# Kernel optimization log

Hardware: AMD Instinct MI355X
Metric: run time of the kernel (lower is better)

## Reference

```python
import jax, jax.numpy as jnp
import numpy as np

D = 512      # input_size == per-head embed_size (wide attention)
H = 8        # num_attn_heads


def setup_inputs() -> dict:
    key = jax.random.key(0)
    ks = jax.random.split(key, 8)
    B, S = 2, 2048
    scale = 1.0 / np.sqrt(D)
    return {
        "Xin_q": jax.random.normal(ks[0], (B, S, D), dtype=jnp.float32),
        "Xin_k": jax.random.normal(ks[1], (B, S, D), dtype=jnp.float32),
        "Xin_v": jax.random.normal(ks[2], (B, S, D), dtype=jnp.float32),
        # per-head projection weights, stored as [H, D_in, D_out] (bias-free)
        "Wq": jax.random.normal(ks[3], (H, D, D), dtype=jnp.float32) * scale,
        "Wk": jax.random.normal(ks[4], (H, D, D), dtype=jnp.float32) * scale,
        "Wv": jax.random.normal(ks[5], (H, D, D), dtype=jnp.float32) * scale,
        # output projection: concat(H*D) -> D, with bias
        "Wz": jax.random.normal(ks[6], (H * D, D), dtype=jnp.float32) * (1.0 / np.sqrt(H * D)),
        "bz": jax.random.normal(ks[7], (D,), dtype=jnp.float32) * 0.01,
    }


def reference(Xin_q, Xin_k, Xin_v, Wq, Wk, Wv, Wz, bz):
    B, Sq, _ = Xin_q.shape
    inv4 = 1.0 / (D ** 0.25)  # each of Q and K scaled by embed_size**(1/4)
    # project all heads at once: [B,H,S,D]
    q = jnp.einsum("bsd,hde->bhse", Xin_q, Wq) * inv4
    k = jnp.einsum("bsd,hde->bhse", Xin_k, Wk) * inv4
    v = jnp.einsum("bsd,hde->bhse", Xin_v, Wv)
    attn = jax.nn.softmax(jnp.einsum("bhqe,bhke->bhqk", q, k), axis=-1)
    z = jnp.einsum("bhqk,bhke->bhqe", attn, v)        # [B,H,S,D]
    # concat heads along last dim (head-major order matches torch.cat over the head loop)
    z = jnp.transpose(z, (0, 2, 1, 3)).reshape(B, Sq, H * D)
    out = z @ Wz + bz                                  # [B,S,D]
    attn_avg = jnp.mean(attn, axis=1)                  # [B,Sq,Skv]
    return out, attn_avg
```

## Files before the change

kernel.cpp:

```cpp
#include <hip/hip_runtime.h>
#include <math.h>

#define BB 2
#define SS 2048
#define D_ 512
#define H_ 8
#define MS (BB * SS)
#define HD (H_ * D_)

typedef short bf16x8 __attribute__((ext_vector_type(8)));
typedef float f32x4 __attribute__((ext_vector_type(4)));

__device__ inline unsigned short f2bf(float f) {
    union { float f; unsigned u; } x{f};
    unsigned r = x.u + 0x7fff + ((x.u >> 16) & 1);
    return (unsigned short)(r >> 16);
}
__device__ inline float bf2f(unsigned short u) {
    union { unsigned u; float f; } x{(unsigned)u << 16};
    return x.f;
}

constexpr size_t SZ_X   = (size_t)MS * D_ * 2;
constexpr size_t SZ_W   = (size_t)H_ * D_ * D_ * 2;
constexpr size_t SZ_WZ  = (size_t)HD * D_ * 2;
constexpr size_t SZ_QK  = (size_t)H_ * MS * D_ * 2;
constexpr size_t SZ_SC  = (size_t)H_ * BB * SS * SS * 2;
constexpr size_t SZ_Z   = (size_t)MS * HD * 2;
constexpr size_t SZ_OP  = (size_t)2 * MS * D_ * 4;
constexpr size_t SZ_LV  = (size_t)H_ * BB * SS * 4;
constexpr size_t OFF_XQ  = 0;
constexpr size_t OFF_XK  = OFF_XQ + SZ_X;
constexpr size_t OFF_XV  = OFF_XK + SZ_X;
constexpr size_t OFF_WQT = OFF_XV + SZ_X;
constexpr size_t OFF_WKT = OFF_WQT + SZ_W;
constexpr size_t OFF_WVT = OFF_WKT + SZ_W;
constexpr size_t OFF_WZT = OFF_WVT + SZ_W;
constexpr size_t OFF_QB  = OFF_WZT + SZ_WZ;
constexpr size_t OFF_KB  = OFF_QB + SZ_QK;
constexpr size_t OFF_VT  = OFF_KB + SZ_QK;
constexpr size_t OFF_SC  = OFF_VT + SZ_QK;
constexpr size_t OFF_Z   = OFF_SC + SZ_SC;
constexpr size_t OFF_OP  = OFF_Z + SZ_Z;
constexpr size_t OFF_LV  = OFF_OP + SZ_OP;
constexpr size_t WS_TOTAL = OFF_LV + SZ_LV;
__device__ __align__(256) unsigned char g_ws[WS_TOTAL];

__device__ inline void gl2lds16(const unsigned short* g, unsigned short* l) {
    __builtin_amdgcn_global_load_lds(
        (const __attribute__((address_space(1))) void*)g,
        (__attribute__((address_space(3))) void*)l, 16, 0, 0);
}

#define BAR() __builtin_amdgcn_s_barrier()
#define PRIO1() __builtin_amdgcn_s_setprio(1)
#define PRIO0() __builtin_amdgcn_s_setprio(0)
#define SCHED0() __builtin_amdgcn_sched_barrier(0)
#define VMW4() asm volatile("s_waitcnt vmcnt(4)" ::: "memory")
#define VMW0() asm volatile("s_waitcnt vmcnt(0)" ::: "memory")

__device__ __forceinline__ void rd_a(const unsigned short* p, int qm, int o0, int o1,
                                     bf16x8 (&Af)[8]) {
#pragma unroll
    for (int fi = 0; fi < 4; fi++) {
        Af[2 * fi]     = *(const bf16x8*)(p + (qm * 64 + fi * 16) * 64 + o0);
        Af[2 * fi + 1] = *(const bf16x8*)(p + (qm * 64 + fi * 16) * 64 + o1);
    }
}
__device__ __forceinline__ void rd_b(const unsigned short* p, int qn, int o0, int o1,
                                     bf16x8 (&Bf)[4]) {
#pragma unroll
    for (int fj = 0; fj < 2; fj++) {
        const int t = qn * 2 + fj;
        Bf[2 * fj]     = *(const bf16x8*)(p + t * 64 + o0);
        Bf[2 * fj + 1] = *(const bf16x8*)(p + t * 64 + o1);
    }
}
__device__ __forceinline__ void mma_q(int qm, int qn, const bf16x8 (&Af)[8],
                                      const bf16x8 (&Bf)[4], f32x4 (&acc)[8][4]) {
#pragma unroll
    for (int fi = 0; fi < 4; fi++)
#pragma unroll
        for (int fj = 0; fj < 2; fj++) {
            acc[qm * 4 + fi][qn * 2 + fj] = __builtin_amdgcn_mfma_f32_16x16x32_bf16(
                Af[2 * fi], Bf[2 * fj], acc[qm * 4 + fi][qn * 2 + fj], 0, 0, 0);
            acc[qm * 4 + fi][qn * 2 + fj] = __builtin_amdgcn_mfma_f32_16x16x32_bf16(
                Af[2 * fi + 1], Bf[2 * fj + 1], acc[qm * 4 + fi][qn * 2 + fj], 0, 0, 0);
        }
}

__global__ __launch_bounds__(512, 2) void gemm256_k(
    const unsigned short* __restrict__ A, const unsigned short* __restrict__ B,
    unsigned short* __restrict__ C, int K, int ldA, int ldB, int ldC,
    long sA1, long sA2, long sB1, long sB2, long sC1, long sC2, int d2,
    float alpha, int doExp, const float* __restrict__ rowScale, long sR1, long sR2,
    int gx, int gy, int gz)
{
    __shared__ unsigned short LA[2][256 * 64];
    __shared__ unsigned short LB[2][256 * 64];
    const int tid = threadIdx.x;
    const int w = tid >> 6, l = tid & 63;
    const int wm = w >> 2, wn = w & 3;

    const int sr = l >> 3;
    const int sqA = (l & 7) ^ sr;
    const int sqB0 = (l & 7) ^ ((w * 4 + (sr >> 2)) & 7);
    const int sqB1 = sqB0 ^ 2;
    const int q = l >> 4, sl = l & 7;
    const int o0 = (q ^ sl) * 8;
    const int o1 = ((q + 4) ^ sl) * 8;
    const unsigned short* pa0 = &LA[0][(wm * 128 + (l & 15)) * 64];
    const unsigned short* pa1 = &LA[1][(wm * 128 + (l & 15)) * 64];
    const unsigned short* pb0 = &LB[0][(wn * 64 + (l & 15) * 4) * 64];
    const unsigned short* pb1 = &LB[1][(wn * 64 + (l & 15) * 4) * 64];

    const int tilesPerZ = gx * gy;
    const int zPerXcd = gz >> 3;
    const int perXcd = zPerXcd * tilesPerZ;
    const int xcd = blockIdx.x & 7, jj = blockIdx.x >> 3;
    const int nT = (perXcd - jj + 31) >> 5;
    const int nK2 = K >> 7;

    auto decode = [&](int idx, const unsigned short*& gA,
                      const unsigned short*& gB0, const unsigned short*& gB1,
                      long& cO, long& rO, int& m0o, int& n0o) {
        const int zl = idx / tilesPerZ;
        const int rem = idx - zl * tilesPerZ;
        const int by = rem / gx;
        const int bx = rem - by * gx;
        const int bz = xcd * zPerXcd + zl;
        const int z1 = bz / d2, z2 = bz - z1 * d2;
        m0o = by * 256; n0o = bx * 256;
        const unsigned short* Az = A + z1 * sA1 + z2 * sA2;
        const unsigned short* Bz = B + z1 * sB1 + z2 * sB2;
        gA  = Az + (long)(m0o + w * 16 + sr) * ldA + sqA * 8;
        gB0 = Bz + (long)(n0o + w * 16 + sr) * ldB + sqB0 * 8;
        gB1 = Bz + (long)(n0o + w * 16 + 8 + sr) * ldB + sqB1 * 8;
        cO = z1 * sC1 + z2 * sC2;
        rO = z1 * sR1 + z2 * sR2;
    };

    const unsigned short *gAc, *gB0c, *gB1c, *gAn, *gB0n, *gB1n;
    long cOff, rsOff, cOffN, rsOffN;
    int m0, n0, m0N, n0N;
    decode(jj, gAc, gB0c, gB1c, cOff, rsOff, m0, n0);
    gAn = gAc; gB0n = gB0c; gB1n = gB1c;
    cOffN = cOff; rsOffN = rsOff; m0N = m0; n0N = n0;

    f32x4 acc[8][4] = {};
    bf16x8 Af[8], Bf0[4], Bf1[4];

#define STG_A(bufi, half, base, t) do { \
    gl2lds16((base) + (long)((half) * 128) * ldA + (long)(t) * 64, \
             &LA[bufi][((half) * 128 + w * 16) * 64]); \
    gl2lds16((base) + (long)((half) * 128 + 8) * ldA + (long)(t) * 64, \
             &LA[bufi][((half) * 128 + w * 16 + 8) * 64]); } while (0)
#define STG_B(bufi, half, b0, b1, t) do { \
    gl2lds16((b0) + (long)((half) * 128) * ldB + (long)(t) * 64, \
             &LB[bufi][((half) * 128 + w * 16) * 64]); \
    gl2lds16((b1) + (long)((half) * 128) * ldB + (long)(t) * 64, \
             &LB[bufi][((half) * 128 + w * 16 + 8) * 64]); } while (0)

    STG_A(0, 0, gAc, 0); STG_A(0, 1, gAc, 0);
    STG_B(0, 0, gB0c, gB1c, 0); STG_B(0, 1, gB0c, gB1c, 0);
    STG_B(1, 0, gB0c, gB1c, 1); STG_B(1, 1, gB0c, gB1c, 1);
    VMW4();
    BAR();
    SCHED0();

    for (int k = 0; k < nT; ++k) {
        const bool hasNext = (k + 1 < nT);
        if (hasNext) decode(jj + (k + 1) * 32, gAn, gB0n, gB1n,
                            cOffN, rsOffN, m0N, n0N);

        for (int u = 0; u < nK2; ++u) {
            const int t1 = 2 * u + 1, t2 = 2 * u + 2, t3 = 2 * u + 3;
            const bool lastU = (u == nK2 - 1);
            const bool stg = !lastU || hasNext;
            const unsigned short* a2 = lastU ? gAn : gAc;
            const unsigned short* b20 = lastU ? gB0n : gB0c;
            const unsigned short* b21 = lastU ? gB1n : gB1c;
            const int tt2 = lastU ? 0 : t2;
            const int tt3 = lastU ? 1 : t3;
            rd_a(pa0, 0, o0, o1, Af);
            rd_b(pb0, 0, o0, o1, Bf0);
            STG_A(1, 0, gAc, t1);
            PRIO1(); mma_q(0, 0, Af, Bf0, acc); PRIO0(); BAR();
            rd_b(pb0, 1, o0, o1, Bf1);
            STG_A(1, 1, gAc, t1);
            PRIO1(); mma_q(0, 1, Af, Bf1, acc); PRIO0(); BAR();
            rd_a(pa0, 1, o0, o1, Af);
            if (stg) STG_B(0, 0, b20, b21, tt2);
            PRIO1(); mma_q(1, 1, Af, Bf1, acc); PRIO0(); BAR();
            if (stg) STG_B(0, 1, b20, b21, tt2);
            PRIO1(); mma_q(1, 0, Af, Bf0, acc); PRIO0();
            if (stg) VMW4(); else VMW0();
            BAR();
            SCHED0();
            rd_a(pa1, 0, o0, o1, Af);
            rd_b(pb1, 0, o0, o1, Bf0);
            if (stg) STG_A(0, 0, a2, tt2);
            PRIO1(); mma_q(0, 0, Af, Bf0, acc); PRIO0(); BAR();
            rd_b(pb1, 1, o0, o1, Bf1);
            if (stg) STG_A(0, 1, a2, tt2);
            PRIO1(); mma_q(0, 1, Af, Bf1, acc); PRIO0(); BAR();
            rd_a(pa1, 1, o0, o1, Af);
            if (stg) STG_B(1, 0, b20, b21, tt3);
            PRIO1(); mma_q(1, 1, Af, Bf1, acc); PRIO0(); BAR();
            if (stg) STG_B(1, 1, b20, b21, tt3);
            PRIO1(); mma_q(1, 0, Af, Bf0, acc); PRIO0();
            if (stg) VMW4(); else VMW0();
            BAR();
            SCHED0();
        }

        {
            const int rowB = m0 + wm * 128 + q * 4;
            const int colB = n0 + wn * 64 + (l & 15) * 4;
            unsigned short* Cp = C + cOff;
#pragma unroll
            for (int mi = 0; mi < 8; mi++) {
#pragma unroll
                for (int rg = 0; rg < 4; rg++) {
                    const int row = rowB + mi * 16 + rg;
                    const float rs = rowScale ? rowScale[rsOff + row] : 1.0f;
                    float v0 = alpha * acc[mi][0][rg];
                    float v1 = alpha * acc[mi][1][rg];
                    float v2 = alpha * acc[mi][2][rg];
                    float v3 = alpha * acc[mi][3][rg];
                    if (doExp) {
                        v0 = __expf(v0); v1 = __expf(v1);
                        v2 = __expf(v2); v3 = __expf(v3);
                    }
                    uint2 pk;
                    pk.x = (unsigned)f2bf(v0 * rs) | ((unsigned)f2bf(v1 * rs) << 16);
                    pk.y = (unsigned)f2bf(v2 * rs) | ((unsigned)f2bf(v3 * rs) << 16);
                    *(uint2*)(Cp + (long)row * ldC + colB) = pk;
                }
            }
        }
#pragma unroll
        for (int mi = 0; mi < 8; mi++)
#pragma unroll
            for (int nj = 0; nj < 4; nj++)
                acc[mi][nj] = (f32x4){0.f, 0.f, 0.f, 0.f};
        gAc = gAn; gB0c = gB0n; gB1c = gB1n;
        cOff = cOffN; rsOff = rsOffN; m0 = m0N; n0 = n0N;
    }
#undef STG_A
#undef STG_B
}

__global__ __launch_bounds__(256) void gemm_bt_k(
    const unsigned short* __restrict__ A, const unsigned short* __restrict__ B,
    void* __restrict__ Cv, int K, int ldA, int ldB, int ldC,
    long sA1, long sA2, long sB1, long sB2, long sC1, long sC2, int d2,
    float alpha, const float* __restrict__ bias, int outBf16, int doExp,
    const float* __restrict__ rowScale, long sR1, long sR2)
{
    __shared__ unsigned short As[128 * 64];
    __shared__ unsigned short Bs[128 * 64];
    const int gx = gridDim.x, gy = gridDim.y, gz = gridDim.z;
    int bx, by, bz;
    if (((gy * gz) & 7) == 0) {
        const long L = blockIdx.x + (long)gx * (blockIdx.y + (long)gy * blockIdx.z);
        const int d = (int)(L & 7);
        const long s = L >> 3;
        bx = (int)(s % gx);
        const long yz = d + 8 * (s / gx);
        by = (int)(yz % gy);
        bz = (int)(yz / gy);
    } else {
        bx = blockIdx.x; by = blockIdx.y; bz = blockIdx.z;
    }
    const int z1 = bz / d2, z2 = bz % d2;
    A += z1 * sA1 + z2 * sA2;
    B += z1 * sB1 + z2 * sB2;
    const long cOff = z1 * sC1 + z2 * sC2;
    const long rsOff = z1 * sR1 + z2 * sR2;
    const int m0 = by * 128, n0 = bx * 128;
    const int tid = threadIdx.x;
    const int w = tid >> 6, l = tid & 63;

    const int sr = l >> 3;
    const int sq = (l & 7) ^ sr;
    const unsigned short* ga = A + (long)(m0 + w * 32 + sr) * ldA + sq * 8;
    const unsigned short* gb = B + (long)(n0 + w * 32 + sr) * ldB + sq * 8;
    unsigned short* laA = As + w * 2048;
    unsigned short* laB = Bs + w * 2048;

    const int wm = w >> 1, wn = w & 1;
    const int q = l >> 4;
    const int sl = l & 7;
    const int mA = wm * 64 + (l & 15);
    const int nB = wn * 64 + (l & 15);
    const int s0 = ((q) ^ sl) * 8;
    const int s1 = ((q + 4) ^ sl) * 8;
    const unsigned short* pa0 = As + mA * 64 + s0;
    const unsigned short* pa1 = As + mA * 64 + s1;
    const unsigned short* pb0 = Bs + nB * 64 + s0;
    const unsigned short* pb1 = Bs + nB * 64 + s1;

    f32x4 acc[4][4] = {};
    for (int kk = 0; kk < K; kk += 64) {
#pragma unroll
        for (int i = 0; i < 4; i++) {
            gl2lds16(ga + (long)i * 8 * ldA, laA + i * 512);
            gl2lds16(gb + (long)i * 8 * ldB, laB + i * 512);
        }
        ga += 64; gb += 64;
        __syncthreads();
        bf16x8 af[4], bf[4];
#pragma unroll
        for (int i = 0; i < 4; i++) {
            af[i] = *(const bf16x8*)(pa0 + i * 1024);
            bf[i] = *(const bf16x8*)(pb0 + i * 1024);
        }
#pragma unroll
        for (int mi = 0; mi < 4; mi++)
#pragma unroll
            for (int ni = 0; ni < 4; ni++)
                acc[mi][ni] = __builtin_amdgcn_mfma_f32_16x16x32_bf16(
                    af[mi], bf[ni], acc[mi][ni], 0, 0, 0);
#pragma unroll
        for (int i = 0; i < 4; i++) {
            af[i] = *(const bf16x8*)(pa1 + i * 1024);
            bf[i] = *(const bf16x8*)(pb1 + i * 1024);
        }
#pragma unroll
        for (int mi = 0; mi < 4; mi++)
#pragma unroll
            for (int ni = 0; ni < 4; ni++)
                acc[mi][ni] = __builtin_amdgcn_mfma_f32_16x16x32_bf16(
                    af[mi], bf[ni], acc[mi][ni], 0, 0, 0);
        __syncthreads();
    }

    const int rowB = m0 + wm * 64 + q * 4;
    const int colB = n0 + wn * 64 + (l & 15);
    if (outBf16) {
        unsigned short* C = (unsigned short*)Cv + cOff;
#pragma unroll
        for (int mi = 0; mi < 4; mi++) {
#pragma unroll
            for (int rg = 0; rg < 4; rg++) {
                const int row = rowB + mi * 16 + rg;
                const float rs = rowScale ? rowScale[rsOff + row] : 1.0f;
#pragma unroll
                for (int ni = 0; ni < 4; ni++) {
                    float v = alpha * acc[mi][ni][rg];
                    if (doExp) v = __expf(v);
                    C[(long)row * ldC + colB + ni * 16] = f2bf(v * rs);
                }
            }
        }
    } else {
        float* C = (float*)Cv + cOff;
#pragma unroll
        for (int ni = 0; ni < 4; ni++) {
            const int col = colB + ni * 16;
            const float bs = bias ? bias[col] : 0.f;
#pragma unroll
            for (int mi = 0; mi < 4; mi++)
#pragma unroll
                for (int rg = 0; rg < 4; rg++)
                    C[(long)(rowB + mi * 16 + rg) * ldC + col] =
                        alpha * acc[mi][ni][rg] + bs;
        }
    }
}

__global__ __launch_bounds__(256) void cvt3_k(
    const float* __restrict__ i0, const float* __restrict__ i1, const float* __restrict__ i2,
    unsigned short* __restrict__ o0, unsigned short* __restrict__ o1,
    unsigned short* __restrict__ o2, long n4)
{
    const float* in = blockIdx.z == 0 ? i0 : (blockIdx.z == 1 ? i1 : i2);
    unsigned short* out = blockIdx.z == 0 ? o0 : (blockIdx.z == 1 ? o1 : o2);
    long i = (long)blockIdx.x * 256 + threadIdx.x;
    if (i >= n4) return;
    float4 v = ((const float4*)in)[i];
    ushort4 o;
    o.x = f2bf(v.x); o.y = f2bf(v.y); o.z = f2bf(v.z); o.w = f2bf(v.w);
    ((ushort4*)out)[i] = o;
}

__global__ __launch_bounds__(256) void transcvt3_k(
    const float* __restrict__ i0, const float* __restrict__ i1, const float* __restrict__ i2,
    unsigned short* __restrict__ o0, unsigned short* __restrict__ o1,
    unsigned short* __restrict__ o2)
{
    __shared__ float t[32][33];
    const int zt = blockIdx.z >> 3, h = blockIdx.z & 7;
    const float* in = (zt == 0 ? i0 : (zt == 1 ? i1 : i2)) + (long)h * D_ * D_;
    unsigned short* out = (zt == 0 ? o0 : (zt == 1 ? o1 : o2)) + (long)h * D_ * D_;
    const int r0 = blockIdx.y * 32, c0 = blockIdx.x * 32;
    const int tr = threadIdx.x >> 5, tc = threadIdx.x & 31;
#pragma unroll
    for (int i = 0; i < 4; i++)
        t[tr + i * 8][tc] = in[(long)(r0 + tr + i * 8) * D_ + c0 + tc];
    __syncthreads();
#pragma unroll
    for (int i = 0; i < 4; i++)
        out[(long)(c0 + tr + i * 8) * D_ + r0 + tc] = f2bf(t[tc][tr + i * 8]);
}

__global__ __launch_bounds__(256) void transcvt_k(
    const float* __restrict__ in, unsigned short* __restrict__ out, int R, int C)
{
    __shared__ float t[32][33];
    const int r0 = blockIdx.y * 32, c0 = blockIdx.x * 32;
    const int tr = threadIdx.x >> 5, tc = threadIdx.x & 31;
#pragma unroll
    for (int i = 0; i < 4; i++)
        t[tr + i * 8][tc] = in[(long)(r0 + tr + i * 8) * C + c0 + tc];
    __syncthreads();
#pragma unroll
    for (int i = 0; i < 4; i++)
        out[(long)(c0 + tr + i * 8) * R + r0 + tc] = f2bf(t[tc][tr + i * 8]);
}

__device__ inline float wred_sum(float v) {
#pragma unroll
    for (int o = 32; o; o >>= 1) v += __shfl_down(v, o);
    return v;
}
__global__ __launch_bounds__(256) void sumavg_k(
    const unsigned short* __restrict__ E, float* __restrict__ avg,
    float* __restrict__ linv)
{
    const int blk = blockIdx.x;
    const int b = blk >> 11, s = blk & (SS - 1);
    const int tid = threadIdx.x;
    const int t0 = tid * 8;
    __shared__ float red[8][4];
    float v[8][8];
    float hs[8];
#pragma unroll
    for (int h = 0; h < H_; h++) {
        const long rowOff = ((long)(h * BB + b) * SS + s) * SS + t0;
        const uint4 u = *(const uint4*)(E + rowOff);
        const unsigned ua[4] = {u.x, u.y, u.z, u.w};
        float sum = 0.f;
#pragma unroll
        for (int i = 0; i < 4; i++) {
            v[h][2 * i]     = bf2f((unsigned short)(ua[i] & 0xffff));
            v[h][2 * i + 1] = bf2f((unsigned short)(ua[i] >> 16));
            sum += v[h][2 * i] + v[h][2 * i + 1];
        }
        hs[h] = sum;
    }
#pragma unroll
    for (int h = 0; h < H_; h++) {
        const float wsum = wred_sum(hs[h]);
        if ((tid & 63) == 0) red[h][tid >> 6] = wsum;
    }
    __syncthreads();
    float inv0, inv1, inv2, inv3, inv4, inv5, inv6, inv7;
    {
        inv0 = 1.0f / (red[0][0] + red[0][1] + red[0][2] + red[0][3]);
        inv1 = 1.0f / (red[1][0] + red[1][1] + red[1][2] + red[1][3]);
        inv2 = 1.0f / (red[2][0] + red[2][1] + red[2][2] + red[2][3]);
        inv3 = 1.0f / (red[3][0] + red[3][1] + red[3][2] + red[3][3]);
        inv4 = 1.0f / (red[4][0] + red[4][1] + red[4][2] + red[4][3]);
        inv5 = 1.0f / (red[5][0] + red[5][1] + red[5][2] + red[5][3]);
        inv6 = 1.0f / (red[6][0] + red[6][1] + red[6][2] + red[6][3]);
        inv7 = 1.0f / (red[7][0] + red[7][1] + red[7][2] + red[7][3]);
    }
    if (tid == 0) {
        linv[(long)(0 * BB + b) * SS + s] = inv0;
        linv[(long)(1 * BB + b) * SS + s] = inv1;
        linv[(long)(2 * BB + b) * SS + s] = inv2;
        linv[(long)(3 * BB + b) * SS + s] = inv3;
        linv[(long)(4 * BB + b) * SS + s] = inv4;
        linv[(long)(5 * BB + b) * SS + s] = inv5;
        linv[(long)(6 * BB + b) * SS + s] = inv6;
        linv[(long)(7 * BB + b) * SS + s] = inv7;
    }
    const float qs[8] = {inv0 * 0.125f, inv1 * 0.125f, inv2 * 0.125f,
                         inv3 * 0.125f, inv4 * 0.125f, inv5 * 0.125f,
                         inv6 * 0.125f, inv7 * 0.125f};
    float av[8] = {};
#pragma unroll
    for (int h = 0; h < H_; h++)
#pragma unroll
        for (int i = 0; i < 8; i++) av[i] += v[h][i] * qs[h];
    const long aOff = ((long)b * SS + s) * SS + t0;
    *(float4*)(avg + aOff) = (float4){av[0], av[1], av[2], av[3]};
    *(float4*)(avg + aOff + 4) = (float4){av[4], av[5], av[6], av[7]};
}

__global__ __launch_bounds__(256) void addbias_k(
    const float* __restrict__ p0, const float* __restrict__ p1,
    const float* __restrict__ bz, float* __restrict__ out)
{
    const long n4 = (long)MS * D_ / 4;
    long i = (long)blockIdx.x * 256 + threadIdx.x;
    if (i >= n4) return;
    const int col4 = (int)((i * 4) & (D_ - 1));
    float4 a = ((const float4*)p0)[i];
    float4 b = ((const float4*)p1)[i];
    float4 c = *(const float4*)(bz + col4);
    float4 o = {a.x + b.x + c.x, a.y + b.y + c.y, a.z + b.z + c.z, a.w + b.w + c.w};
    ((float4*)out)[i] = o;
}

extern "C" void kernel_launch(void* const* d_in, const int* in_sizes, int n_in,
                              void* d_out, int out_size, void* d_ws, size_t ws_size,
                              hipStream_t stream)
{
    const float* Xq = (const float*)d_in[0];
    const float* Xk = (const float*)d_in[1];
    const float* Xv = (const float*)d_in[2];
    const float* Wq = (const float*)d_in[3];
    const float* Wk = (const float*)d_in[4];
    const float* Wv = (const float*)d_in[5];
    const float* Wz = (const float*)d_in[6];
    const float* bz = (const float*)d_in[7];

    float* out      = (float*)d_out;
    float* attn_avg = out + (long)MS * D_;

    unsigned char* ws = nullptr;
    (void)hipGetSymbolAddress((void**)&ws, HIP_SYMBOL(g_ws));
    unsigned short* Xbq = (unsigned short*)(ws + OFF_XQ);
    unsigned short* Xbk = (unsigned short*)(ws + OFF_XK);
    unsigned short* Xbv = (unsigned short*)(ws + OFF_XV);
    unsigned short* Wqt = (unsigned short*)(ws + OFF_WQT);
    unsigned short* Wkt = (unsigned short*)(ws + OFF_WKT);
    unsigned short* Wvt = (unsigned short*)(ws + OFF_WVT);
    unsigned short* Wzt = (unsigned short*)(ws + OFF_WZT);
    unsigned short* qb  = (unsigned short*)(ws + OFF_QB);
    unsigned short* vT  = (unsigned short*)(ws + OFF_VT);
    unsigned short* scb = (unsigned short*)(ws + OFF_SC);
    unsigned short* zal = (unsigned short*)(ws + OFF_Z);
    float*          opp = (float*)(ws + OFF_OP);
    float*          linv = (float*)(ws + OFF_LV);

    const float inv4 = 1.0f / powf((float)D_, 0.25f);

    const long n4x = (long)MS * D_ / 4;
    cvt3_k<<<dim3((n4x + 255) / 256, 1, 3), 256, 0, stream>>>(
        Xq, Xk, Xv, Xbq, Xbk, Xbv, n4x);
    transcvt3_k<<<dim3(16, 16, 24), 256, 0, stream>>>(Wq, Wk, Wv, Wqt, Wkt, Wvt);
    transcvt_k<<<dim3(16, 128, 1), 256, 0, stream>>>(Wz, Wzt, HD, D_);

    gemm256_k<<<dim3(256), 512, 0, stream>>>(
        Xbq, Wqt, qb, D_, D_, D_, D_,
        (long)MS * D_, 0, (long)H_ * D_ * D_, (long)D_ * D_,
        (long)H_ * MS * D_, (long)MS * D_, 8, inv4, 0, nullptr, 0, 0,
        2, 16, 16);
    gemm256_k<<<dim3(256), 512, 0, stream>>>(
        Wvt, Xbv, vT, D_, D_, D_, SS,
        (long)D_ * D_, 0, 0, (long)SS * D_, (long)2 * D_ * SS, (long)D_ * SS, 2,
        1.0f, 0, nullptr, 0, 0,
        8, 2, 16);

    gemm256_k<<<dim3(256), 512, 0, stream>>>(
        qb, qb + (long)H_ * MS * D_, scb, D_, D_, D_, SS,
        (long)MS * D_, (long)SS * D_, (long)MS * D_, (long)SS * D_,
        (long)2 * SS * SS, (long)SS * SS, 2, 1.0f, 1, nullptr, 0, 0,
        8, 8, 16);

    sumavg_k<<<dim3(BB * SS), 256, 0, stream>>>(scb, attn_avg, linv);

    gemm256_k<<<dim3(256), 512, 0, stream>>>(
        scb, vT, zal, SS, SS, SS, HD,
        (long)2 * SS * SS, (long)SS * SS, (long)2 * D_ * SS, (long)D_ * SS,
        512, (long)SS * HD, 2, 1.0f, 0,
        linv, (long)BB * SS, (long)SS,
        2, 8, 16);

    gemm_bt_k<<<dim3(4, 32, 2), 256, 0, stream>>>(
        zal, Wzt, opp, HD / 2, HD, HD, D_,
        0, 2048, 0, 2048, 0, (long)MS * D_, 2, 1.0f, nullptr, 0, 0, nullptr, 0, 0);
    const long n4o = (long)MS * D_ / 4;
    addbias_k<<<dim3((n4o + 255) / 256), 256, 0, stream>>>(
        opp, opp + (long)MS * D_, bz, out);
}
```

Before: 441.2 us.

## Route output projection through pipelined 256-tile GEMM with 8-way split-K

Drops the simple 128-tile gemm_bt_k for the output projection. The 256x256 software-pipelined gemm256_k now handles it, gaining an fp32 output path and splitting K=4096 into 8 partial slices, one per head. A new addbias8_k sums the 8 partials and adds the bias. The sumavg kernel also uses nontemporal loads and stores for the streamed score and attn_avg data. The tradeoff is a larger fp32 partial buffer, since the reduce kernel now reads 8 partial outputs instead of 2.

Result: faster. 427.3 us (-3.1%).

```diff
diff --git a/kernel.cpp b/kernel.cpp
--- a/kernel.cpp
+++ b/kernel.cpp
@@ -10,6 +10,9 @@
 
 typedef short bf16x8 __attribute__((ext_vector_type(8)));
 typedef float f32x4 __attribute__((ext_vector_type(4)));
+typedef unsigned u32x2 __attribute__((ext_vector_type(2)));
+typedef unsigned u32x4 __attribute__((ext_vector_type(4)));
+typedef unsigned short u16x4 __attribute__((ext_vector_type(4)));
 
 __device__ inline unsigned short f2bf(float f) {
     union { float f; unsigned u; } x{f};
@@ -27,7 +30,7 @@
 constexpr size_t SZ_QK  = (size_t)H_ * MS * D_ * 2;
 constexpr size_t SZ_SC  = (size_t)H_ * BB * SS * SS * 2;
 constexpr size_t SZ_Z   = (size_t)MS * HD * 2;
-constexpr size_t SZ_OP  = (size_t)2 * MS * D_ * 4;
+constexpr size_t SZ_OP  = (size_t)8 * MS * D_ * 4;
 constexpr size_t SZ_LV  = (size_t)H_ * BB * SS * 4;
 constexpr size_t OFF_XQ  = 0;
 constexpr size_t OFF_XK  = OFF_XQ + SZ_X;
@@ -91,10 +94,10 @@
 
 __global__ __launch_bounds__(512, 2) void gemm256_k(
     const unsigned short* __restrict__ A, const unsigned short* __restrict__ B,
-    unsigned short* __restrict__ C, int K, int ldA, int ldB, int ldC,
+    void* __restrict__ Cv, int K, int ldA, int ldB, int ldC,
     long sA1, long sA2, long sB1, long sB2, long sC1, long sC2, int d2,
     float alpha, int doExp, const float* __restrict__ rowScale, long sR1, long sR2,
-    int gx, int gy, int gz)
+    int gx, int gy, int gz, int outBf16)
 {
     __shared__ unsigned short LA[2][256 * 64];
     __shared__ unsigned short LB[2][256 * 64];
@@ -217,7 +220,6 @@
         {
             const int rowB = m0 + wm * 128 + q * 4;
             const int colB = n0 + wn * 64 + (l & 15) * 4;
-            unsigned short* Cp = C + cOff;
 #pragma unroll
             for (int mi = 0; mi < 8; mi++) {
 #pragma unroll
@@ -232,10 +234,17 @@
                         v0 = __expf(v0); v1 = __expf(v1);
                         v2 = __expf(v2); v3 = __expf(v3);
                     }
-                    uint2 pk;
-                    pk.x = (unsigned)f2bf(v0 * rs) | ((unsigned)f2bf(v1 * rs) << 16);
-                    pk.y = (unsigned)f2bf(v2 * rs) | ((unsigned)f2bf(v3 * rs) << 16);
-                    *(uint2*)(Cp + (long)row * ldC + colB) = pk;
+                    if (outBf16) {
+                        unsigned short* Cp = (unsigned short*)Cv + cOff;
+                        uint2 pk;
+                        pk.x = (unsigned)f2bf(v0 * rs) | ((unsigned)f2bf(v1 * rs) << 16);
+                        pk.y = (unsigned)f2bf(v2 * rs) | ((unsigned)f2bf(v3 * rs) << 16);
+                        *(uint2*)(Cp + (long)row * ldC + colB) = pk;
+                    } else {
+                        float* Cf = (float*)Cv + cOff;
+                        f32x4 pk = {v0 * rs, v1 * rs, v2 * rs, v3 * rs};
+                        *(f32x4*)(Cf + (long)row * ldC + colB) = pk;
+                    }
                 }
             }
         }
@@ -249,125 +258,6 @@
     }
 #undef STG_A
 #undef STG_B
-}
-
-__global__ __launch_bounds__(256) void gemm_bt_k(
-    const unsigned short* __restrict__ A, const unsigned short* __restrict__ B,
-    void* __restrict__ Cv, int K, int ldA, int ldB, int ldC,
-    long sA1, long sA2, long sB1, long sB2, long sC1, long sC2, int d2,
-    float alpha, const float* __restrict__ bias, int outBf16, int doExp,
-    const float* __restrict__ rowScale, long sR1, long sR2)
-{
-    __shared__ unsigned short As[128 * 64];
-    __shared__ unsigned short Bs[128 * 64];
-    const int gx = gridDim.x, gy = gridDim.y, gz = gridDim.z;
-    int bx, by, bz;
-    if (((gy * gz) & 7) == 0) {
-        const long L = blockIdx.x + (long)gx * (blockIdx.y + (long)gy * blockIdx.z);
-        const int d = (int)(L & 7);
-        const long s = L >> 3;
-        bx = (int)(s % gx);
-        const long yz = d + 8 * (s / gx);
-        by = (int)(yz % gy);
-        bz = (int)(yz / gy);
-    } else {
-        bx = blockIdx.x; by = blockIdx.y; bz = blockIdx.z;
-    }
-    const int z1 = bz / d2, z2 = bz % d2;
-    A += z1 * sA1 + z2 * sA2;
-    B += z1 * sB1 + z2 * sB2;
-    const long cOff = z1 * sC1 + z2 * sC2;
-    const long rsOff = z1 * sR1 + z2 * sR2;
-    const int m0 = by * 128, n0 = bx * 128;
-    const int tid = threadIdx.x;
-    const int w = tid >> 6, l = tid & 63;
-
-    const int sr = l >> 3;
-    const int sq = (l & 7) ^ sr;
-    const unsigned short* ga = A + (long)(m0 + w * 32 + sr) * ldA + sq * 8;
-    const unsigned short* gb = B + (long)(n0 + w * 32 + sr) * ldB + sq * 8;
-    unsigned short* laA = As + w * 2048;
-    unsigned short* laB = Bs + w * 2048;
-
-    const int wm = w >> 1, wn = w & 1;
-    const int q = l >> 4;
-    const int sl = l & 7;
-    const int mA = wm * 64 + (l & 15);
-    const int nB = wn * 64 + (l & 15);
-    const int s0 = ((q) ^ sl) * 8;
-    const int s1 = ((q + 4) ^ sl) * 8;
-    const unsigned short* pa0 = As + mA * 64 + s0;
-    const unsigned short* pa1 = As + mA * 64 + s1;
-    const unsigned short* pb0 = Bs + nB * 64 + s0;
-    const unsigned short* pb1 = Bs + nB * 64 + s1;
-
-    f32x4 acc[4][4] = {};
-    for (int kk = 0; kk < K; kk += 64) {
-#pragma unroll
-        for (int i = 0; i < 4; i++) {
-            gl2lds16(ga + (long)i * 8 * ldA, laA + i * 512);
-            gl2lds16(gb + (long)i * 8 * ldB, laB + i * 512);
-        }
-        ga += 64; gb += 64;
-        __syncthreads();
-        bf16x8 af[4], bf[4];
-#pragma unroll
-        for (int i = 0; i < 4; i++) {
-            af[i] = *(const bf16x8*)(pa0 + i * 1024);
-            bf[i] = *(const bf16x8*)(pb0 + i * 1024);
-        }
-#pragma unroll
-        for (int mi = 0; mi < 4; mi++)
-#pragma unroll
-            for (int ni = 0; ni < 4; ni++)
-                acc[mi][ni] = __builtin_amdgcn_mfma_f32_16x16x32_bf16(
-                    af[mi], bf[ni], acc[mi][ni], 0, 0, 0);
-#pragma unroll
-        for (int i = 0; i < 4; i++) {
-            af[i] = *(const bf16x8*)(pa1 + i * 1024);
-            bf[i] = *(const bf16x8*)(pb1 + i * 1024);
-        }
-#pragma unroll
-        for (int mi = 0; mi < 4; mi++)
-#pragma unroll
-            for (int ni = 0; ni < 4; ni++)
-                acc[mi][ni] = __builtin_amdgcn_mfma_f32_16x16x32_bf16(
-                    af[mi], bf[ni], acc[mi][ni], 0, 0, 0);
-        __syncthreads();
-    }
-
-    const int rowB = m0 + wm * 64 + q * 4;
-    const int colB = n0 + wn * 64 + (l & 15);
-    if (outBf16) {
-        unsigned short* C = (unsigned short*)Cv + cOff;
-#pragma unroll
-        for (int mi = 0; mi < 4; mi++) {
-#pragma unroll
-            for (int rg = 0; rg < 4; rg++) {
-                const int row = rowB + mi * 16 + rg;
-                const float rs = rowScale ? rowScale[rsOff + row] : 1.0f;
-#pragma unroll
-                for (int ni = 0; ni < 4; ni++) {
-                    float v = alpha * acc[mi][ni][rg];
-                    if (doExp) v = __expf(v);
-                    C[(long)row * ldC + colB + ni * 16] = f2bf(v * rs);
-                }
-            }
-        }
-    } else {
-        float* C = (float*)Cv + cOff;
-#pragma unroll
-        for (int ni = 0; ni < 4; ni++) {
-            const int col = colB + ni * 16;
-            const float bs = bias ? bias[col] : 0.f;
-#pragma unroll
-            for (int mi = 0; mi < 4; mi++)
-#pragma unroll
-                for (int rg = 0; rg < 4; rg++)
-                    C[(long)(rowB + mi * 16 + rg) * ldC + col] =
-                        alpha * acc[mi][ni][rg] + bs;
-        }
-    }
 }
 
 __global__ __launch_bounds__(256) void cvt3_k(
@@ -439,7 +329,7 @@
 #pragma unroll
     for (int h = 0; h < H_; h++) {
         const long rowOff = ((long)(h * BB + b) * SS + s) * SS + t0;
-        const uint4 u = *(const uint4*)(E + rowOff);
+        const u32x4 u = __builtin_nontemporal_load((const u32x4*)(E + rowOff));
         const unsigned ua[4] = {u.x, u.y, u.z, u.w};
         float sum = 0.f;
 #pragma unroll
@@ -456,17 +346,14 @@
         if ((tid & 63) == 0) red[h][tid >> 6] = wsum;
     }
     __syncthreads();
-    float inv0, inv1, inv2, inv3, inv4, inv5, inv6, inv7;
-    {
-        inv0 = 1.0f / (red[0][0] + red[0][1] + red[0][2] + red[0][3]);
-        inv1 = 1.0f / (red[1][0] + red[1][1] + red[1][2] + red[1][3]);
-        inv2 = 1.0f / (red[2][0] + red[2][1] + red[2][2] + red[2][3]);
-        inv3 = 1.0f / (red[3][0] + red[3][1] + red[3][2] + red[3][3]);
-        inv4 = 1.0f / (red[4][0] + red[4][1] + red[4][2] + red[4][3]);
-        inv5 = 1.0f / (red[5][0] + red[5][1] + red[5][2] + red[5][3]);
-        inv6 = 1.0f / (red[6][0] + red[6][1] + red[6][2] + red[6][3]);
-        inv7 = 1.0f / (red[7][0] + red[7][1] + red[7][2] + red[7][3]);
-    }
+    float inv0 = 1.0f / (red[0][0] + red[0][1] + red[0][2] + red[0][3]);
+    float inv1 = 1.0f / (red[1][0] + red[1][1] + red[1][2] + red[1][3]);
+    float inv2 = 1.0f / (red[2][0] + red[2][1] + red[2][2] + red[2][3]);
+    float inv3 = 1.0f / (red[3][0] + red[3][1] + red[3][2] + red[3][3]);
+    float inv4 = 1.0f / (red[4][0] + red[4][1] + red[4][2] + red[4][3]);
+    float inv5 = 1.0f / (red[5][0] + red[5][1] + red[5][2] + red[5][3]);
+    float inv6 = 1.0f / (red[6][0] + red[6][1] + red[6][2] + red[6][3]);
+    float inv7 = 1.0f / (red[7][0] + red[7][1] + red[7][2] + red[7][3]);
     if (tid == 0) {
         linv[(long)(0 * BB + b) * SS + s] = inv0;
         linv[(long)(1 * BB + b) * SS + s] = inv1;
@@ -486,23 +373,28 @@
 #pragma unroll
         for (int i = 0; i < 8; i++) av[i] += v[h][i] * qs[h];
     const long aOff = ((long)b * SS + s) * SS + t0;
-    *(float4*)(avg + aOff) = (float4){av[0], av[1], av[2], av[3]};
-    *(float4*)(avg + aOff + 4) = (float4){av[4], av[5], av[6], av[7]};
-}
-
-__global__ __launch_bounds__(256) void addbias_k(
-    const float* __restrict__ p0, const float* __restrict__ p1,
-    const float* __restrict__ bz, float* __restrict__ out)
+    f32x4 a0 = {av[0], av[1], av[2], av[3]};
+    f32x4 a1 = {av[4], av[5], av[6], av[7]};
+    __builtin_nontemporal_store(a0, (f32x4*)(avg + aOff));
+    __builtin_nontemporal_store(a1, (f32x4*)(avg + aOff + 4));
+}
+
+__global__ __launch_bounds__(256) void addbias8_k(
+    const float* __restrict__ p, const float* __restrict__ bz,
+    float* __restrict__ out)
 {
     const long n4 = (long)MS * D_ / 4;
     long i = (long)blockIdx.x * 256 + threadIdx.x;
     if (i >= n4) return;
     const int col4 = (int)((i * 4) & (D_ - 1));
-    float4 a = ((const float4*)p0)[i];
-    float4 b = ((const float4*)p1)[i];
     float4 c = *(const float4*)(bz + col4);
-    float4 o = {a.x + b.x + c.x, a.y + b.y + c.y, a.z + b.z + c.z, a.w + b.w + c.w};
-    ((float4*)out)[i] = o;
+    f32x4 s = {c.x, c.y, c.z, c.w};
+#pragma unroll
+    for (int j = 0; j < 8; j++) {
+        float4 a = ((const float4*)(p + (long)j * MS * D_))[i];
+        s.x += a.x; s.y += a.y; s.z += a.z; s.w += a.w;
+    }
+    __builtin_nontemporal_store(s, (f32x4*)out + i);
 }
 
 extern "C" void kernel_launch(void* const* d_in, const int* in_sizes, int n_in,
@@ -549,18 +441,18 @@
         Xbq, Wqt, qb, D_, D_, D_, D_,
         (long)MS * D_, 0, (long)H_ * D_ * D_, (long)D_ * D_,
         (long)H_ * MS * D_, (long)MS * D_, 8, inv4, 0, nullptr, 0, 0,
-        2, 16, 16);
+        2, 16, 16, 1);
     gemm256_k<<<dim3(256), 512, 0, stream>>>(
         Wvt, Xbv, vT, D_, D_, D_, SS,
         (long)D_ * D_, 0, 0, (long)SS * D_, (long)2 * D_ * SS, (long)D_ * SS, 2,
         1.0f, 0, nullptr, 0, 0,
-        8, 2, 16);
+        8, 2, 16, 1);
 
     gemm256_k<<<dim3(256), 512, 0, stream>>>(
         qb, qb + (long)H_ * MS * D_, scb, D_, D_, D_, SS,
         (long)MS * D_, (long)SS * D_, (long)MS * D_, (long)SS * D_,
         (long)2 * SS * SS, (long)SS * SS, 2, 1.0f, 1, nullptr, 0, 0,
-        8, 8, 16);
+        8, 8, 16, 1);
 
     sumavg_k<<<dim3(BB * SS), 256, 0, stream>>>(scb, attn_avg, linv);
 
@@ -569,12 +461,12 @@
         (long)2 * SS * SS, (long)SS * SS, (long)2 * D_ * SS, (long)D_ * SS,
         512, (long)SS * HD, 2, 1.0f, 0,
         linv, (long)BB * SS, (long)SS,
-        2, 8, 16);
-
-    gemm_bt_k<<<dim3(4, 32, 2), 256, 0, stream>>>(
-        zal, Wzt, opp, HD / 2, HD, HD, D_,
-        0, 2048, 0, 2048, 0, (long)MS * D_, 2, 1.0f, nullptr, 0, 0, nullptr, 0, 0);
+        2, 8, 16, 1);
+
+    gemm256_k<<<dim3(256), 512, 0, stream>>>(
+        zal, Wzt, opp, D_, HD, HD, D_,
+        0, 512, 0, 512, 0, (long)MS * D_, 8, 1.0f, 0, nullptr, 0, 0,
+        2, 16, 8, 0);
     const long n4o = (long)MS * D_ / 4;
-    addbias_k<<<dim3((n4o + 255) / 256), 256, 0, stream>>>(
-        opp, opp + (long)MS * D_, bz, out);
-}
+    addbias8_k<<<dim3((n4o + 255) / 256), 256, 0, stream>>>(opp, bz, out);
+}
```
